# Performance work log

Hardware: AMD Instinct MI355X
Metric: run time of the kernel (lower is better)

Reference implementation:

```python
import jax, jax.numpy as jnp
import numpy as np

# Module constants (from init_kwargs)
TRUNC = (32, 32, 32)
OUT_SIZE = (32, 32, 32)
HOMOMORPHIC = False


def dct2_ortho_mat(N):
    """Orthonormal DCT-II matrix C of shape [N, N]; y = C @ x along an axis.
    IDCT (DCT-III ortho) is C.T since C is orthogonal."""
    n = jnp.arange(N, dtype=jnp.float32)          # sample index
    k = n[:, None]                                 # frequency index
    C = jnp.cos(jnp.pi * (2.0 * n + 1.0) * k / (2.0 * N))
    scale = jnp.where(k == 0, jnp.sqrt(1.0 / N), jnp.sqrt(2.0 / N))
    return (C * scale).astype(jnp.float32)


def _transform3d(x, Cd, Ch, Cw):
    # Apply separable 1D transforms along D, H, W axes of [B, C, D, H, W].
    x = jnp.einsum('kd,bcdhw->bckhw', Cd, x)
    x = jnp.einsum('kh,bcdhw->bcdkw', Ch, x)
    x = jnp.einsum('kw,bcdhw->bcdhk', Cw, x)
    return x


def setup_inputs() -> dict:
    key = jax.random.key(0)
    x = jax.random.normal(key, (4, 32, 64, 64, 64), dtype=jnp.float32)
    return {"x": x}


def reference(x) -> jnp.ndarray:
    B, C, D, H, W = x.shape
    if HOMOMORPHIC:
        x = jnp.log(x + 1e-6)

    # 3D DCT-II (ortho) along D, H, W
    Cd, Ch, Cw = dct2_ortho_mat(D), dct2_ortho_mat(H), dct2_ortho_mat(W)
    x_dct = _transform3d(x, Cd, Ch, Cw)

    # Crop low frequencies to `truncation`, zero-pad up to `output_size`
    t0, t1, t2 = TRUNC
    o0, o1, o2 = OUT_SIZE
    x_crop = x_dct[:, :, :t0, :t1, :t2]
    x_pad = jnp.pad(x_crop, ((0, 0), (0, 0), (0, o0 - t0), (0, o1 - t1), (0, o2 - t2)))

    # 3D IDCT (DCT-III ortho) = transpose of the ortho DCT-II matrix
    Id, Ih, Iw = dct2_ortho_mat(o0).T, dct2_ortho_mat(o1).T, dct2_ortho_mat(o2).T
    out = _transform3d(x_pad, Id, Ih, Iw)

    if HOMOMORPHIC:
        out = jnp.exp(out)
    return out
```

## Files before the change

kernel.cpp:

```cpp
#include <hip/hip_runtime.h>
#include <hip/hip_bf16.h>
#include <math.h>
#include <stdint.h>


#define PI_F 3.14159265358979323846f

typedef __attribute__((ext_vector_type(4))) float f32x4;
typedef __attribute__((ext_vector_type(8))) short bf16x8;

union U16x8 { uint4 q; bf16x8 v; uint32_t w[4]; };

__device__ __forceinline__ uint32_t pk(float a, float b) {
    union { __hip_bfloat162 h; uint32_t u; } c;
    c.h = __float22bfloat162_rn(make_float2(a, b));
    return c.u;
}

__device__ __forceinline__ unsigned short bf16r(float x) {
    union { float f; uint32_t u; } c; c.f = x;
    uint32_t r = (c.u + 0x7FFFu + ((c.u >> 16) & 1u)) >> 16;
    return (unsigned short)r;
}

__device__ __forceinline__ float Aelem(int i, int d) {
    const float s1 = sqrtf(1.0f / 32.0f), s2 = sqrtf(2.0f / 32.0f);
    const float t1 = sqrtf(1.0f / 64.0f), t2 = sqrtf(2.0f / 64.0f);
    float acc = 0.f;
    for (int k = 0; k < 32; ++k) {
        int n1 = ((2 * i + 1) * k) & 127;
        int n2 = ((2 * d + 1) * k) & 255;
        float c1 = cosf((float)n1 * (PI_F / 64.0f));
        float c2 = cosf((float)n2 * (PI_F / 128.0f));
        acc += ((k == 0) ? s1 : s2) * ((k == 0) ? t1 : t2) * c1 * c2;
    }
    return acc;
}

__global__ __launch_bounds__(256) void build_tables(float* __restrict__ At,
                                                    unsigned short* __restrict__ F) {
    int e = blockIdx.x * 256 + threadIdx.x;
    if (e < 2048) {
        int d = e >> 5, i = e & 31;
        At[e] = Aelem(i, d);
    } else if (e < 4096) {
        int f = e - 2048;
        int jj = f & 7, lane = (f >> 3) & 63, tk = f >> 9;
        int tt = tk >> 1, kt = tk & 1;
        int row = tt * 16 + (lane & 15);
        int col = kt * 32 + ((lane >> 4) << 3) + jj;
        F[f] = bf16r(Aelem(row, col));
    }
}

__global__ __launch_bounds__(256, 4) void k_hw(const float* __restrict__ x,
                                               const unsigned short* __restrict__ F,
                                               unsigned short* __restrict__ w1b) {
    __shared__ unsigned short Ut[4][2048];

    const int t = threadIdx.x;
    const int wv = t >> 6, ln = t & 63;
    const int lm = ln & 15, lg = ln >> 4;
    const size_t slab = (size_t)blockIdx.x * 4 + wv;

    bf16x8 Ff[2][2];
    {
        const uint4* fp = (const uint4*)F;
        #pragma unroll
        for (int tt = 0; tt < 2; ++tt)
            #pragma unroll
            for (int kt = 0; kt < 2; ++kt) {
                U16x8 u; u.q = fp[(tt * 2 + kt) * 64 + ln];
                Ff[tt][kt] = u.v;
            }
    }

    const float* xs = x + slab * 4096;
    uint4 raw[16];
    #pragma unroll
    for (int mt = 0; mt < 4; ++mt)
        #pragma unroll
        for (int kt = 0; kt < 2; ++kt) {
            const uint4* p = (const uint4*)(xs + (mt * 16 + lm) * 64 + kt * 32 + (lg << 3));
            raw[(mt * 2 + kt) * 2 + 0] = p[0];
            raw[(mt * 2 + kt) * 2 + 1] = p[1];
        }

    f32x4 accu[4][2];
    #pragma unroll
    for (int mt = 0; mt < 4; ++mt)
        #pragma unroll
        for (int nt = 0; nt < 2; ++nt)
            accu[mt][nt] = (f32x4){0.f, 0.f, 0.f, 0.f};

    #pragma unroll
    for (int mt = 0; mt < 4; ++mt) {
        #pragma unroll
        for (int kt = 0; kt < 2; ++kt) {
            const float* f0 = (const float*)&raw[(mt * 2 + kt) * 2];
            U16x8 xf;
            #pragma unroll
            for (int e = 0; e < 4; ++e)
                xf.w[e] = pk(f0[2 * e], f0[2 * e + 1]);
            #pragma unroll
            for (int nt = 0; nt < 2; ++nt)
                accu[mt][nt] = __builtin_amdgcn_mfma_f32_16x16x32_bf16(
                    xf.v, Ff[nt][kt], accu[mt][nt], 0, 0, 0);
        }
    }

    unsigned short* ut = Ut[wv];
    #pragma unroll
    for (int mt = 0; mt < 4; ++mt)
        #pragma unroll
        for (int nt = 0; nt < 2; ++nt) {
            int lo = nt * 16 + lm;
            int h0 = mt * 16 + (lg << 2);
            uint32_t w0 = pk(accu[mt][nt][0], accu[mt][nt][1]);
            uint32_t w1v = pk(accu[mt][nt][2], accu[mt][nt][3]);
            uint32_t byte = (uint32_t)(lo * 128 + 2 * h0);
            byte ^= (uint32_t)((lo & 7) << 4);
            *(uint2*)((char*)ut + byte) = make_uint2(w0, w1v);
        }
    __builtin_amdgcn_wave_barrier();

    f32x4 acco[2][2];
    #pragma unroll
    for (int mt = 0; mt < 2; ++mt)
        #pragma unroll
        for (int nt = 0; nt < 2; ++nt)
            acco[mt][nt] = (f32x4){0.f, 0.f, 0.f, 0.f};

    #pragma unroll
    for (int mt = 0; mt < 2; ++mt) {
        #pragma unroll
        for (int kt = 0; kt < 2; ++kt) {
            int lo = mt * 16 + lm;
            uint32_t byte = (uint32_t)(lo * 128 + kt * 64 + (lg << 4));
            byte ^= (uint32_t)((lo & 7) << 4);
            bf16x8 uf = *(const bf16x8*)((const char*)ut + byte);
            #pragma unroll
            for (int nt = 0; nt < 2; ++nt)
                acco[mt][nt] = __builtin_amdgcn_mfma_f32_16x16x32_bf16(
                    uf, Ff[nt][kt], acco[mt][nt], 0, 0, 0);
        }
    }

    #pragma unroll
    for (int mt = 0; mt < 2; ++mt)
        #pragma unroll
        for (int nt = 0; nt < 2; ++nt) {
            uint32_t u0 = pk(acco[mt][nt][0], acco[mt][nt][1]);
            uint32_t u1 = pk(acco[mt][nt][2], acco[mt][nt][3]);
            int j  = nt * 16 + lm;
            int l0 = mt * 16 + (lg << 2);
            *(uint2*)(w1b + slab * 1024 + j * 32 + l0) = make_uint2(u0, u1);
        }
}

__global__ __launch_bounds__(256) void k_d(const unsigned short* __restrict__ w1b,
                                           const float* __restrict__ At,
                                           float* __restrict__ out) {
    const int t = threadIdx.x;
    const int bc = blockIdx.x >> 3;
    const int kh = (blockIdx.x >> 2) & 1;
    const int q  = blockIdx.x & 3;
    const int p  = q * 256 + t;
    const unsigned short* src = w1b + (size_t)bc * 65536 + p;
    float acc[16];
    #pragma unroll
    for (int k = 0; k < 16; ++k) acc[k] = 0.f;
    #pragma unroll 8
    for (int d = 0; d < 64; ++d) {
        uint32_t u = (uint32_t)src[d * 1024];
        float v = __uint_as_float(u << 16);
        const float* arow = At + d * 32 + kh * 16;
        #pragma unroll
        for (int k = 0; k < 16; ++k) acc[k] += arow[k] * v;
    }
    float* dst = out + (size_t)bc * 32768 + (size_t)kh * 16384 + p;
    #pragma unroll
    for (int k = 0; k < 16; ++k) dst[k * 1024] = acc[k];
}

extern "C" void kernel_launch(void* const* d_in, const int* in_sizes, int n_in,
                              void* d_out, int out_size, void* d_ws, size_t ws_size,
                              hipStream_t stream) {
    const float* x = (const float*)d_in[0];
    float* out = (float*)d_out;

    float* At           = (float*)d_ws;
    unsigned short* F   = (unsigned short*)((char*)d_ws + 8192);
    unsigned short* w1b = (unsigned short*)((char*)d_ws + 16384);

    build_tables<<<16, 256, 0, stream>>>(At, F);
    k_hw<<<2048, 256, 0, stream>>>(x, F, w1b);
    k_d<<<1024, 256, 0, stream>>>(w1b, At, out);
}
```

Measured before the change: 45.81 us.

## Stage input slab through LDS via direct global-to-LDS loads with swizzle

The k_hw kernel now copies each wave's 16 KB input slab straight into shared memory with global_load_lds, using contiguous 16-byte-per-lane accesses and an XOR swizzle, instead of scattered per-lane register loads. The MFMA operands are then read back from LDS. The goal is fully coalesced global reads and lower register pressure. In exchange, LDS use per block rises to 80 KB, the launch-bounds occupancy hint is dropped, and there is a full vmcnt wait before any compute starts, so blocks per CU may fall.

New measurement: 45.93 us. Within noise of the previous version (+0.3%).

```diff
diff --git a/kernel.cpp b/kernel.cpp
--- a/kernel.cpp
+++ b/kernel.cpp
@@ -53,15 +53,18 @@
     }
 }
 
-__global__ __launch_bounds__(256, 4) void k_hw(const float* __restrict__ x,
-                                               const unsigned short* __restrict__ F,
-                                               unsigned short* __restrict__ w1b) {
-    __shared__ unsigned short Ut[4][2048];
+__global__ __launch_bounds__(256) void k_hw(const float* __restrict__ x,
+                                            const unsigned short* __restrict__ F,
+                                            unsigned short* __restrict__ w1b) {
+    __shared__ __align__(16) char lds_all[4][20480];
 
     const int t = threadIdx.x;
     const int wv = t >> 6, ln = t & 63;
     const int lm = ln & 15, lg = ln >> 4;
     const size_t slab = (size_t)blockIdx.x * 4 + wv;
+
+    char* Xs = lds_all[wv];
+    unsigned short* ut = (unsigned short*)(lds_all[wv] + 16384);
 
     bf16x8 Ff[2][2];
     {
@@ -75,16 +78,18 @@
             }
     }
 
-    const float* xs = x + slab * 4096;
-    uint4 raw[16];
-    #pragma unroll
-    for (int mt = 0; mt < 4; ++mt)
-        #pragma unroll
-        for (int kt = 0; kt < 2; ++kt) {
-            const uint4* p = (const uint4*)(xs + (mt * 16 + lm) * 64 + kt * 32 + (lg << 3));
-            raw[(mt * 2 + kt) * 2 + 0] = p[0];
-            raw[(mt * 2 + kt) * 2 + 1] = p[1];
-        }
+    const char* xb = (const char*)(x + slab * 4096);
+    #pragma unroll
+    for (int s = 0; s < 16; ++s) {
+        uint32_t d = (uint32_t)(s * 1024 + ln * 16);
+        uint32_t g = d ^ (((d >> 8) & 7u) << 5);
+        __builtin_amdgcn_global_load_lds(
+            (const __attribute__((address_space(1))) uint32_t*)(xb + g),
+            (__attribute__((address_space(3))) uint32_t*)(Xs + s * 1024),
+            16, 0, 0);
+    }
+    asm volatile("s_waitcnt vmcnt(0)" ::: "memory");
+    __builtin_amdgcn_sched_barrier(0);
 
     f32x4 accu[4][2];
     #pragma unroll
@@ -97,11 +102,15 @@
     for (int mt = 0; mt < 4; ++mt) {
         #pragma unroll
         for (int kt = 0; kt < 2; ++kt) {
-            const float* f0 = (const float*)&raw[(mt * 2 + kt) * 2];
+            uint32_t a = (uint32_t)((mt * 16 + lm) * 256 + kt * 128 + lg * 32);
+            a ^= ((a >> 8) & 7u) << 5;
+            const float4* fp4 = (const float4*)(Xs + a);
+            float4 A0 = fp4[0], A1 = fp4[1];
             U16x8 xf;
-            #pragma unroll
-            for (int e = 0; e < 4; ++e)
-                xf.w[e] = pk(f0[2 * e], f0[2 * e + 1]);
+            xf.w[0] = pk(A0.x, A0.y);
+            xf.w[1] = pk(A0.z, A0.w);
+            xf.w[2] = pk(A1.x, A1.y);
+            xf.w[3] = pk(A1.z, A1.w);
             #pragma unroll
             for (int nt = 0; nt < 2; ++nt)
                 accu[mt][nt] = __builtin_amdgcn_mfma_f32_16x16x32_bf16(
@@ -109,7 +118,6 @@
         }
     }
 
-    unsigned short* ut = Ut[wv];
     #pragma unroll
     for (int mt = 0; mt < 4; ++mt)
         #pragma unroll
```
